# Kernel optimization log

Measured on AMD Instinct MI355X. Metric: run time of the kernel, lower is better.

Reference implementation:

```python
import jax, jax.numpy as jnp
from jax import lax
import numpy as np

# dims
V, D, T = 30000, 300, 24          # vocab, glove dim, seq len
H = 256                            # tweet_out_size == z_dim
NT, NU = 6000, 4000                # tweet nodes, user nodes
N = NT + NU
F, Z = 512, 256                    # user_feat_size, z_dim
E = 80000
B = 2000                           # batch_size (source tweets)
H1, H2, HEADS = 64, 100, 8
NEG = 0.2                          # GATConv default negative_slope


def setup_inputs() -> dict:
    k = jax.random.split(jax.random.key(0), 32)
    r = lambda i, shape, s=0.05: (s * jax.random.normal(k[i], shape)).astype(jnp.float32)
    return {
        "user_text": jax.random.randint(k[0], (B, T), 0, V),
        "user_feats": jax.random.normal(k[1], (NU, F), jnp.float32),
        "graph_node_features": jax.random.randint(k[2], (NT, T), 0, V),
        "graph_edge_index": jax.random.randint(k[3], (2, E), 0, N),
        "tweet_emb": r(4, (V, D), 0.1),
        "w_ih0": r(5, (3 * H, D)), "w_hh0": r(6, (3 * H, H)),
        "b_ih0": r(7, (3 * H,)), "b_hh0": r(8, (3 * H,)),
        "w_ih1": r(9, (3 * H, H)), "w_hh1": r(10, (3 * H, H)),
        "b_ih1": r(11, (3 * H,)), "b_hh1": r(12, (3 * H,)),
        "h0": r(13, (2, NT, H), 1.0),
        "w_mu": r(14, (Z, F)), "b_mu": r(15, (Z,)),
        "w_lv": r(16, (Z, F)), "b_lv": r(17, (Z,)),
        "w_dec": r(18, (F, Z)), "b_dec": r(19, (F,)),
        "vae_eps": r(20, (NU, Z), 1.0),
        "w1": r(21, (H, HEADS * H1)), "a_src1": r(22, (HEADS, H1)),
        "a_dst1": r(23, (HEADS, H1)), "b1": r(24, (HEADS * H1,)),
        "w2": r(25, (HEADS * H1, H2)), "a_src2": r(26, (1, H2)),
        "a_dst2": r(27, (1, H2)), "b2": r(28, (H2,)),
    }


def _gru_layer(x_seq, h0, w_ih, w_hh, b_ih, b_hh):
    # x_seq: [T, B, in]; torch nn.GRU gate math
    def step(h, x):
        gi = x @ w_ih.T + b_ih
        gh = h @ w_hh.T + b_hh
        i_r, i_z, i_n = jnp.split(gi, 3, axis=-1)
        h_r, h_z, h_n = jnp.split(gh, 3, axis=-1)
        r = jax.nn.sigmoid(i_r + h_r)
        z = jax.nn.sigmoid(i_z + h_z)
        n = jnp.tanh(i_n + r * h_n)
        hn = (1.0 - z) * n + z * h
        return hn, hn
    h_last, out = lax.scan(step, h0, x_seq)
    return out, h_last


def _gat(x, src, dst, w, a_src, a_dst, bias, heads, out_ch, concat):
    # PyG GATConv (eval mode, self-loops already appended)
    n = x.shape[0]
    xp = (x @ w).reshape(n, heads, out_ch)          # [N, H, C]
    as_n = (xp * a_src).sum(-1)                     # [N, H]
    ad_n = (xp * a_dst).sum(-1)
    e = jax.nn.leaky_relu(as_n[src] + ad_n[dst], NEG)          # [E, H]
    emax = jax.ops.segment_max(e, dst, num_segments=n)         # edge-softmax over dst
    ee = jnp.exp(e - emax[dst])
    denom = jax.ops.segment_sum(ee, dst, num_segments=n)
    alpha = ee / denom[dst]
    out = jax.ops.segment_sum(xp[src] * alpha[:, :, None], dst, num_segments=n)
    out = out.reshape(n, heads * out_ch) if concat else out.mean(axis=1)
    return out + bias


def reference(user_text, user_feats, graph_node_features, graph_edge_index,
              tweet_emb, w_ih0, w_hh0, b_ih0, b_hh0, w_ih1, w_hh1, b_ih1, b_hh1,
              h0, w_mu, b_mu, w_lv, b_lv, w_dec, b_dec, vae_eps,
              w1, a_src1, a_dst1, b1, w2, a_src2, a_dst2, b2):
    # --- VAE user embedding ---
    mu = user_feats @ w_mu.T + b_mu
    logvar = user_feats @ w_lv.T + b_lv
    z = mu + jnp.exp(0.5 * logvar) * vae_eps        # reparameterized latent
    rec = z @ w_dec.T + b_dec
    kl_loss = (-0.5 * (1.0 + logvar - mu**2 - jnp.exp(logvar)).sum(-1)).mean()
    rec_loss = ((rec - user_feats) ** 2).mean()
    # --- tweet encoder: embedding lookup + 2-layer GRU ---
    xe = tweet_emb[graph_node_features].transpose(1, 0, 2)     # [T, NT, D]
    out0, _ = _gru_layer(xe, h0[0], w_ih0, w_hh0, b_ih0, b_hh0)
    _, hn = _gru_layer(out0, h0[1], w_ih1, w_hh1, b_ih1, b_hh1)  # [NT, H]
    # --- assemble node features: source tweets, users, other tweets ---
    x_in = jnp.concatenate([hn[:B], z, hn[B:]], axis=0)        # [N, H]
    loops = jnp.arange(x_in.shape[0])
    src = jnp.concatenate([graph_edge_index[0], loops])
    dst = jnp.concatenate([graph_edge_index[1], loops])
    x1 = _gat(x_in, src, dst, w1, a_src1, a_dst1, b1, HEADS, H1, True)
    x2 = _gat(x1, src, dst, w2, a_src2, a_dst2, b2, 1, H2, False)
    return x2, kl_loss, rec_loss
```

## Files before the change

### kernel.cpp

```cpp
#include <hip/hip_runtime.h>

#define V_ 30000
#define D_ 300
#define DP_ 320
#define T_ 24
#define H_ 256
#define NT_ 6000
#define NU_ 4000
#define N_ 10000
#define F_ 512
#define Z_ 256
#define E_ 80000
#define B_ 2000
#define H1_ 64
#define H2_ 100
#define HEADS_ 8
#define E2_ (E_ + N_)

typedef __bf16 bf16_t;
typedef bf16_t bf16x8 __attribute__((ext_vector_type(8)));
typedef float  f32x4  __attribute__((ext_vector_type(4)));

__device__ __forceinline__ void gll16(const bf16_t* g, bf16_t* l)
{
    __builtin_amdgcn_global_load_lds(
        (const __attribute__((address_space(1))) void*)g,
        (__attribute__((address_space(3))) void*)l, 16, 0, 0);
}

struct GCfg {
    const bf16_t* A; const bf16_t* B; const float* bias;
    float* Cf; bf16_t* Cb; int M, N, K, ldc;
    const int* gtok; int t0;
};

template<bool OUTBF>
__global__ __launch_bounds__(256) void mfma_gemm(GCfg g0, GCfg g1)
{
    const GCfg g = blockIdx.z ? g1 : g0;
    __shared__ __align__(16) bf16_t SMEM[16384];
    const int tid  = (int)threadIdx.x;
    const int wave = tid >> 6, lane = tid & 63;
    const int quad = lane >> 4, l16 = lane & 15;
    const int mq = (wave & 1) * 64, nq = (wave >> 1) * 64;

    int bx = (int)blockIdx.x, by = (int)blockIdx.y;
    {
        int gx = (int)gridDim.x, total = gx * (int)gridDim.y;
        if ((total & 7) == 0) {
            int L = by * gx + bx;
            int F = (L & 7) * (total >> 3) + (L >> 3);
            bx = F % gx;
            by = F / gx;
        }
    }
    const int mbase = by * 128, nbase = bx * 128;
    const int M = g.M, N = g.N, K = g.K, ldc = g.ldc;

    const bf16_t* agp[2];
    const bf16_t* bgp[2];
#pragma unroll
    for (int j = 0; j < 2; j++) {
        int i = wave * 128 + j * 64 + lane;
        int c = i >> 7, row = i & 127;
        int r = mbase + row; if (r >= M) r = M - 1;
        int src = g.gtok ? g.gtok[(r % NT_) * T_ + g.t0 + (r / NT_)] : r;
        agp[j] = g.A + (size_t)src * K + c * 8;
        int rb = nbase + row; if (rb >= N) rb = N - 1;
        bgp[j] = g.B + (size_t)rb * K + c * 8;
    }

    f32x4 acc[4][4];
#pragma unroll
    for (int mi = 0; mi < 4; mi++)
#pragma unroll
        for (int ni = 0; ni < 4; ni++) acc[mi][ni] = (f32x4){0.f, 0.f, 0.f, 0.f};

    auto stage = [&](int b, int k0) {
        bf16_t* ab = SMEM + b * 4096 + wave * 1024;
        bf16_t* bb = SMEM + 8192 + b * 4096 + wave * 1024;
        gll16(agp[0] + k0, ab);
        gll16(agp[1] + k0, ab + 512);
        gll16(bgp[0] + k0, bb);
        gll16(bgp[1] + k0, bb + 512);
    };

    const int niter = K >> 5;
    stage(0, 0);
    for (int ks = 0; ks < niter; ks++) {
        __syncthreads();
        if (ks + 1 < niter) stage((ks + 1) & 1, (ks + 1) * 32);
        const bf16_t* Ab = SMEM + (ks & 1) * 4096;
        const bf16_t* Bb = SMEM + 8192 + (ks & 1) * 4096;
        bf16x8 afr[4], bfr[4];
#pragma unroll
        for (int mi = 0; mi < 4; mi++)
            afr[mi] = *(const bf16x8*)(Ab + (size_t)(quad * 128 + mq + mi * 16 + l16) * 8);
#pragma unroll
        for (int ni = 0; ni < 4; ni++)
            bfr[ni] = *(const bf16x8*)(Bb + (size_t)(quad * 128 + nq + ni * 16 + l16) * 8);
#pragma unroll
        for (int mi = 0; mi < 4; mi++)
#pragma unroll
            for (int ni = 0; ni < 4; ni++)
                acc[mi][ni] = __builtin_amdgcn_mfma_f32_16x16x32_bf16(
                    afr[mi], bfr[ni], acc[mi][ni], 0, 0, 0);
    }

    if (OUTBF) {
        __syncthreads();
#pragma unroll
        for (int ni = 0; ni < 4; ni++) {
            int colc = nq + ni * 16 + l16;
            float bv = g.bias ? g.bias[nbase + colc] : 0.f;
            int cc = colc >> 3, off = colc & 7;
#pragma unroll
            for (int mi = 0; mi < 4; mi++)
#pragma unroll
                for (int r = 0; r < 4; r++) {
                    int row = mq + mi * 16 + quad * 4 + r;
                    int sw = (row ^ (row >> 3)) & 7;
                    SMEM[row * 128 + ((cc ^ sw) << 3) + off] =
                        (bf16_t)(acc[mi][ni][r] + bv);
                }
        }
        __syncthreads();
        {
            int row = tid >> 1, seg = tid & 1;
            int sw = (row ^ (row >> 3)) & 7;
            int growr = mbase + row;
            if (growr < M) {
#pragma unroll
                for (int q = 0; q < 8; q++) {
                    int cc = seg * 8 + q;
                    bf16x8 v = *(const bf16x8*)(SMEM + row * 128 + ((cc ^ sw) << 3));
                    *(bf16x8*)(g.Cb + (size_t)growr * ldc + nbase + cc * 8) = v;
                }
            }
        }
    } else {
#pragma unroll
        for (int ni = 0; ni < 4; ni++) {
            int col = nbase + nq + ni * 16 + l16;
            if (col >= N) continue;
            float bv = g.bias ? g.bias[col] : 0.f;
#pragma unroll
            for (int mi = 0; mi < 4; mi++)
#pragma unroll
                for (int r = 0; r < 4; r++) {
                    int row = mbase + mq + mi * 16 + quad * 4 + r;
                    if (row >= M) continue;
                    g.Cf[(size_t)row * ldc + col] = acc[mi][ni][r] + bv;
                }
        }
    }
}

struct MegaLay {
    const bf16_t* temb;
    const int*    gnf;
    const bf16_t* wih0;
    const bf16_t* whh0;
    const bf16_t* wih1;
    const bf16_t* whh1;
    const float *bih0, *bhh0, *bih1, *bhh1;
    const bf16_t* h0in;
    const bf16_t* h1in;
    bf16_t*       h1out;
};

__device__ __forceinline__ float rcp_(float x)
{
    float r;
    asm("v_rcp_f32 %0, %1" : "=v"(r) : "v"(x));
    return r;
}
__device__ __forceinline__ float sigm_(float x)
{
    return rcp_(1.f + __expf(-x));
}
__device__ __forceinline__ float tanh_(float x)
{
    x = fminf(fmaxf(x, -15.f), 15.f);
    float t = __expf(2.f * x);
    return 1.f - 2.f * rcp_(t + 1.f);
}

#define HSW(Hb, row, byte) ((char*)(Hb) + ((((row) * 512) + (byte)) ^ (((row) & 7) << 4)))

__global__ __launch_bounds__(512, 2) void gru_mega(MegaLay L)
{
    __shared__ __align__(16) bf16_t H0L[8192];
    __shared__ __align__(16) bf16_t H1L[8192];
    __shared__ __align__(16) bf16_t XE[20480];
    __shared__ int TOK[768];
    const int tid  = (int)threadIdx.x;
    const int wv   = tid >> 6, lane = tid & 63;
    const int quad = lane >> 4, l16 = lane & 15;
    const int row0 = (int)blockIdx.x * 32;

    for (int i = tid; i < 768; i += 512) {
        int gi = row0 * T_ + i; if (gi >= NT_ * T_) gi = NT_ * T_ - 1;
        TOK[i] = L.gnf[gi];
    }
#pragma unroll
    for (int i = 0; i < 2; i++) {
        int idx  = i * 512 + tid;
        int rowl = idx >> 5, seg = idx & 31;
        int grow = row0 + rowl; if (grow >= NT_) grow = NT_ - 1;
        *(bf16x8*)HSW(H0L, rowl, seg * 16) =
            *(const bf16x8*)(L.h0in + (size_t)grow * H_ + seg * 8);
        *(bf16x8*)HSW(H1L, rowl, seg * 16) =
            *(const bf16x8*)(L.h1in + (size_t)grow * H_ + seg * 8);
    }

    float brz0[2][2], bni0[2], bnh0[2], brz1[2][2], bni1[2], bnh1[2];
#pragma unroll
    for (int jj = 0; jj < 2; jj++) {
        int col = wv * 32 + jj * 16 + l16;
        brz0[0][jj] = L.bih0[col] + L.bhh0[col];
        brz0[1][jj] = L.bih0[256 + col] + L.bhh0[256 + col];
        bni0[jj]    = L.bih0[512 + col];
        bnh0[jj]    = L.bhh0[512 + col];
        brz1[0][jj] = L.bih1[col] + L.bhh1[col];
        brz1[1][jj] = L.bih1[256 + col] + L.bhh1[256 + col];
        bni1[jj]    = L.bih1[512 + col];
        bnh1[jj]    = L.bhh1[512 + col];
    }

    auto gather = [&](int t) {
        bf16_t* xb = XE + (t & 1) * 10240;
#pragma unroll
        for (int k = 0; k < 3; k++) {
            int i = wv + k * 8;
            if (i < 20) {
                int flat = i * 64 + lane;
                int row  = flat / 40;
                int s    = flat - row * 40;
                int c4   = s ^ (row & 7);
                int tok  = TOK[row * T_ + t];
                gll16(L.temb + (size_t)tok * DP_ + c4 * 8, xb + i * 512 + lane * 8);
            }
        }
    };

    auto run_gemm = [&](auto&& loadA, const bf16_t* W, int nks,
                        f32x4 (&arz)[2][2][2], f32x4 (&an)[2][2]) {
#pragma unroll 2
        for (int ks = 0; ks < nks; ks++) {
            bf16x8 afr[2];
            loadA(afr, ks);
            bf16x8 bfr[3][2];
#pragma unroll
            for (int g = 0; g < 3; g++)
#pragma unroll
                for (int jj = 0; jj < 2; jj++)
                    bfr[g][jj] = *(const bf16x8*)(W +
                        (((size_t)(g * 16 + wv * 2 + jj) * nks + ks) << 9) + lane * 8);
#pragma unroll
            for (int m = 0; m < 2; m++)
#pragma unroll
                for (int jj = 0; jj < 2; jj++) {
                    arz[m][0][jj] = __builtin_amdgcn_mfma_f32_16x16x32_bf16(
                        afr[m], bfr[0][jj], arz[m][0][jj], 0, 0, 0);
                    arz[m][1][jj] = __builtin_amdgcn_mfma_f32_16x16x32_bf16(
                        afr[m], bfr[1][jj], arz[m][1][jj], 0, 0, 0);
                    an[m][jj] = __builtin_amdgcn_mfma_f32_16x16x32_bf16(
                        afr[m], bfr[2][jj], an[m][jj], 0, 0, 0);
                }
        }
    };

    __syncthreads();
    gather(0);

    for (int t = 0; t < T_; t++) {
        __syncthreads();
        if (t + 1 < T_) gather(t + 1);

        f32x4 arz[2][2][2], an_i[2][2], an_h[2][2];
#pragma unroll
        for (int m = 0; m < 2; m++)
#pragma unroll
            for (int jj = 0; jj < 2; jj++) {
                arz[m][0][jj] = (f32x4){0.f, 0.f, 0.f, 0.f};
                arz[m][1][jj] = (f32x4){0.f, 0.f, 0.f, 0.f};
                an_i[m][jj]   = (f32x4){0.f, 0.f, 0.f, 0.f};
                an_h[m][jj]   = (f32x4){0.f, 0.f, 0.f, 0.f};
            }

        {
            const bf16_t* xb = XE + (t & 1) * 10240;
            run_gemm([&](bf16x8* afr, int ks) {
#pragma unroll
                for (int m = 0; m < 2; m++) {
                    int row = m * 16 + l16;
                    afr[m] = *(const bf16x8*)(xb + row * DP_ +
                               (((ks * 4 + quad) ^ (row & 7)) << 3));
                }
            }, L.wih0, 10, arz, an_i);
            run_gemm([&](bf16x8* afr, int ks) {
#pragma unroll
                for (int m = 0; m < 2; m++)
                    afr[m] = *(const bf16x8*)HSW(H0L, m * 16 + l16,
                                                 ks * 64 + quad * 16);
            }, L.whh0, 8, arz, an_h);
        }
        __syncthreads();

#pragma unroll
        for (int m = 0; m < 2; m++)
#pragma unroll
            for (int jj = 0; jj < 2; jj++) {
                int col = wv * 32 + jj * 16 + l16;
#pragma unroll
                for (int r = 0; r < 4; r++) {
                    int rowl = m * 16 + quad * 4 + r;
                    float hold = (float)*(const bf16_t*)HSW(H0L, rowl, col * 2);
                    float rg = sigm_(arz[m][0][jj][r] + brz0[0][jj]);
                    float zg = sigm_(arz[m][1][jj][r] + brz0[1][jj]);
                    float ng = tanh_(an_i[m][jj][r] + bni0[jj] +
                                     rg * (an_h[m][jj][r] + bnh0[jj]));
                    *(bf16_t*)HSW(H0L, rowl, col * 2) =
                        (bf16_t)((1.f - zg) * ng + zg * hold);
                }
            }
        __syncthreads();

#pragma unroll
        for (int m = 0; m < 2; m++)
#pragma unroll
            for (int jj = 0; jj < 2; jj++) {
                arz[m][0][jj] = (f32x4){0.f, 0.f, 0.f, 0.f};
                arz[m][1][jj] = (f32x4){0.f, 0.f, 0.f, 0.f};
                an_i[m][jj]   = (f32x4){0.f, 0.f, 0.f, 0.f};
                an_h[m][jj]   = (f32x4){0.f, 0.f, 0.f, 0.f};
            }
        run_gemm([&](bf16x8* afr, int ks) {
#pragma unroll
            for (int m = 0; m < 2; m++)
                afr[m] = *(const bf16x8*)HSW(H0L, m * 16 + l16,
                                             ks * 64 + quad * 16);
        }, L.wih1, 8, arz, an_i);
        run_gemm([&](bf16x8* afr, int ks) {
#pragma unroll
            for (int m = 0; m < 2; m++)
                afr[m] = *(const bf16x8*)HSW(H1L, m * 16 + l16,
                                             ks * 64 + quad * 16);
        }, L.whh1, 8, arz, an_h);
        __syncthreads();

#pragma unroll
        for (int m = 0; m < 2; m++)
#pragma unroll
            for (int jj = 0; jj < 2; jj++) {
                int col = wv * 32 + jj * 16 + l16;
#pragma unroll
                for (int r = 0; r < 4; r++) {
                    int rowl = m * 16 + quad * 4 + r;
                    float hold = (float)*(const bf16_t*)HSW(H1L, rowl, col * 2);
                    float rg = sigm_(arz[m][0][jj][r] + brz1[0][jj]);
                    float zg = sigm_(arz[m][1][jj][r] + brz1[1][jj]);
                    float ng = tanh_(an_i[m][jj][r] + bni1[jj] +
                                     rg * (an_h[m][jj][r] + bnh1[jj]));
                    *(bf16_t*)HSW(H1L, rowl, col * 2) =
                        (bf16_t)((1.f - zg) * ng + zg * hold);
                }
            }
    }

    __syncthreads();
#pragma unroll
    for (int i = 0; i < 2; i++) {
        int idx  = i * 512 + tid;
        int rowl = idx >> 5, seg = idx & 31;
        int grow = row0 + rowl;
        if (grow < NT_) {
            bf16x8 v = *(const bf16x8*)HSW(H1L, rowl, seg * 16);
            *(bf16x8*)(L.h1out + (size_t)grow * H_ + seg * 8) = v;
        }
    }
}

struct SegD { const float* src; bf16_t* dst; int rows, cin, cout, transp; };
struct PrepArgs { SegD seg[11]; long long base[12]; int nseg; long long total; };

__global__ void prep_kern(PrepArgs pa)
{
    long long stride = (long long)gridDim.x * blockDim.x;
    for (long long i = (long long)blockIdx.x * blockDim.x + threadIdx.x;
         i < pa.total; i += stride) {
        int k = 0;
        while (k + 1 < pa.nseg && i >= pa.base[k + 1]) k++;
        long long local = i - pa.base[k];
        SegD sg = pa.seg[k];
        float v;
        if (sg.transp == 2) {
            int nks  = sg.cout >> 5;
            int o    = (int)local;
            int e    = o & 7;
            int lane = (o >> 3) & 63;
            int rest = o >> 9;
            int ks   = rest % nks;
            int gcb  = rest / nks;
            int r    = (gcb >> 4) * 256 + (gcb & 15) * 16 + (lane & 15);
            int kk   = ks * 32 + (lane >> 4) * 8 + e;
            v = (kk < sg.cin) ? sg.src[(size_t)r * sg.cin + kk] : 0.f;
        } else {
            int r = (int)(local / sg.cout);
            int c = (int)(local - (long long)r * sg.cout);
            if (sg.transp) v = sg.src[(size_t)c * sg.rows + r];
            else           v = (c < sg.cin) ? sg.src[(size_t)r * sg.cin + c] : 0.f;
        }
        sg.dst[local] = (bf16_t)v;
    }
}

__global__ void init_all(const float* __restrict__ h0in, bf16_t* __restrict__ h0b,
                         bf16_t* __restrict__ h1b,
                         int* __restrict__ deg, int* __restrict__ dcnt,
                         float* __restrict__ loss2, float* __restrict__ b_ml,
                         const float* __restrict__ b_mu, const float* __restrict__ b_lv)
{
    int i = blockIdx.x * blockDim.x + threadIdx.x;
    if (i < NT_ * H_) {
        h0b[i] = (bf16_t)h0in[i];
        h1b[i] = (bf16_t)h0in[NT_ * H_ + i];
    }
    if (i < N_) { deg[i] = 0; dcnt[i] = 0; }
    if (i < 2 * Z_) b_ml[i] = (i < Z_) ? b_mu[i] : b_lv[i - Z_];
    if (i < 2) loss2[i] = 0.f;
}

__device__ __forceinline__ void edge_sd(const int* __restrict__ ei, int e, int& s, int& d)
{
    if (e < E_) { s = ei[e]; d = ei[E_ + e]; }
    else        { s = d = e - E_; }
}

__global__ void csr_hist(const int* __restrict__ ei, int* __restrict__ deg)
{
    int e = blockIdx.x * blockDim.x + threadIdx.x;
    if (e >= E2_) return;
    int s, d; edge_sd(ei, e, s, d);
    atomicAdd(deg + d, 1);
}

__global__ void csr_scan(const int* __restrict__ deg, int* __restrict__ rowptr)
{
    __shared__ int buf[256];
    __shared__ int carry;
    int tid = (int)threadIdx.x;
    if (tid == 0) { carry = 0; rowptr[0] = 0; }
    __syncthreads();
    for (int c0 = 0; c0 < N_; c0 += 256) {
        int i = c0 + tid;
        buf[tid] = (i < N_) ? deg[i] : 0;
        __syncthreads();
        for (int off = 1; off < 256; off <<= 1) {
            int t = (tid >= off) ? buf[tid - off] : 0;
            __syncthreads();
            buf[tid] += t;
            __syncthreads();
        }
        if (i < N_) rowptr[i + 1] = carry + buf[tid];
        __syncthreads();
        if (tid == 255) carry += buf[255];
        __syncthreads();
    }
}

__global__ void csr_scatter(const int* __restrict__ ei, const int* __restrict__ rowptr,
                            int* __restrict__ dcnt, int* __restrict__ csrc)
{
    int e = blockIdx.x * blockDim.x + threadIdx.x;
    if (e >= E2_) return;
    int s, d; edge_sd(ei, e, s, d);
    int pos = rowptr[d] + atomicAdd(dcnt + d, 1);
    csrc[pos] = s;
}

__global__ __launch_bounds__(256) void vae_z_kl(
    const float* __restrict__ ml, const float* __restrict__ eps,
    bf16_t* __restrict__ z_out, float* __restrict__ kl_out)
{
    float t = 0.f;
    int stride = (int)gridDim.x * 256;
    for (int idx = blockIdx.x * 256 + threadIdx.x; idx < NU_ * Z_; idx += stride) {
        int row = idx >> 8, c = idx & 255;
        float m = ml[(size_t)row * 512 + c];
        float l = ml[(size_t)row * 512 + 256 + c];
        float el = expf(l);
        z_out[idx] = (bf16_t)(m + expf(0.5f * l) * eps[idx]);
        t += -0.5f * (1.f + l - m * m - el);
    }
    __shared__ float red[256];
    red[threadIdx.x] = t;
    __syncthreads();
    for (int s = 128; s > 0; s >>= 1) {
        if ((int)threadIdx.x < s) red[threadIdx.x] += red[threadIdx.x + s];
        __syncthreads();
    }
    if (threadIdx.x == 0) atomicAdd(kl_out, red[0] * (1.f / NU_));
}

__global__ __launch_bounds__(256) void rec_loss_kern(
    const float* __restrict__ rec, const float* __restrict__ uf,
    float* __restrict__ loss_out)
{
    float t = 0.f;
    int stride = (int)gridDim.x * 256;
    for (int idx = blockIdx.x * 256 + threadIdx.x; idx < NU_ * F_; idx += stride) {
        float d = rec[idx] - uf[idx];
        t += d * d;
    }
    __shared__ float red[256];
    red[threadIdx.x] = t;
    __syncthreads();
    for (int s = 128; s > 0; s >>= 1) {
        if ((int)threadIdx.x < s) red[threadIdx.x] += red[threadIdx.x + s];
        __syncthreads();
    }
    if (threadIdx.x == 0) atomicAdd(loss_out, red[0] * (1.f / (NU_ * F_)));
}

__global__ void assemble_xin(const bf16_t* __restrict__ h1, bf16_t* __restrict__ x_in)
{
    int idx = blockIdx.x * blockDim.x + threadIdx.x;
    if (idx >= NT_ * H_) return;
    int row = idx >> 8, col = idx & 255;
    int dst = (row < B_) ? row : (row + NU_);
    x_in[(size_t)dst * H_ + col] = h1[idx];
}

__global__ void gat_attn_coef_bf(const bf16_t* __restrict__ xp,
                                 const float* __restrict__ a_src,
                                 const float* __restrict__ a_dst,
                                 float* __restrict__ asn, float* __restrict__ adn,
                                 int heads, int C)
{
    int i = blockIdx.x * blockDim.x + threadIdx.x;
    if (i >= N_ * heads) return;
    int node = i / heads, h = i - node * heads;
    const bf16_t* x = xp + (size_t)(node * heads + h) * C;
    float s = 0.f, d = 0.f;
    for (int c8 = 0; c8 < C; c8 += 8) {
        bf16x8 v = *(const bf16x8*)(x + c8);
#pragma unroll
        for (int j = 0; j < 8; j++) {
            float vv = (float)v[j];
            s += vv * a_src[h * C + c8 + j];
            d += vv * a_dst[h * C + c8 + j];
        }
    }
    asn[i] = s;
    adn[i] = d;
}

__global__ void gat_attn_coef(const float* __restrict__ xp, const float* __restrict__ a_src,
                              const float* __restrict__ a_dst, float* __restrict__ asn,
                              float* __restrict__ adn, int heads, int C)
{
    int i = blockIdx.x * blockDim.x + threadIdx.x;
    if (i >= N_ * heads) return;
    int node = i / heads, h = i - node * heads;
    const float* x = xp + (size_t)(node * heads + h) * C;
    float s = 0.f, d = 0.f;
    for (int c = 0; c < C; c++) {
        float v = x[c];
        s += v * a_src[h * C + c];
        d += v * a_dst[h * C + c];
    }
    asn[i] = s;
    adn[i] = d;
}

__global__ __launch_bounds__(256) void gat_agg1(
    const int* __restrict__ rowptr, const int* __restrict__ csrc,
    const float* __restrict__ asn, const float* __restrict__ adn,
    const bf16_t* __restrict__ xp, const float* __restrict__ bias,
    bf16_t* __restrict__ x1out)
{
    int d = blockIdx.x;
    int tid = (int)threadIdx.x;
    int beg = rowptr[d], end = rowptr[d + 1];
    int h0 = tid >> 6, h1 = h0 + 4;
    float ad0 = adn[d * 8 + h0], ad1 = adn[d * 8 + h1];
    float mx0 = -1e30f, mx1 = -1e30f;
    for (int e = beg; e < end; e++) {
        int s = csrc[e];
        float l0 = asn[s * 8 + h0] + ad0; l0 = (l0 > 0.f) ? l0 : 0.2f * l0;
        float l1 = asn[s * 8 + h1] + ad1; l1 = (l1 > 0.f) ? l1 : 0.2f * l1;
        mx0 = fmaxf(mx0, l0); mx1 = fmaxf(mx1, l1);
    }
    float den0 = 0.f, den1 = 0.f, acc0 = 0.f, acc1 = 0.f;
    for (int e = beg; e < end; e++) {
        int s = csrc[e];
        float l0 = asn[s * 8 + h0] + ad0; l0 = (l0 > 0.f) ? l0 : 0.2f * l0;
        float l1 = asn[s * 8 + h1] + ad1; l1 = (l1 > 0.f) ? l1 : 0.2f * l1;
        float p0 = expf(l0 - mx0), p1 = expf(l1 - mx1);
        den0 += p0; den1 += p1;
        acc0 += p0 * (float)xp[(size_t)s * 512 + tid];
        acc1 += p1 * (float)xp[(size_t)s * 512 + 256 + tid];
    }
    x1out[(size_t)d * 512 + tid]       = (bf16_t)(bias[tid] + acc0 / den0);
    x1out[(size_t)d * 512 + 256 + tid] = (bf16_t)(bias[256 + tid] + acc1 / den1);
}

__global__ __launch_bounds__(256) void gat_agg2(
    const int* __restrict__ rowptr, const int* __restrict__ csrc,
    const float* __restrict__ asn, const float* __restrict__ adn,
    const float* __restrict__ xp, const float* __restrict__ bias,
    float* __restrict__ outp)
{
    int d = blockIdx.x * 4 + ((int)threadIdx.x >> 6);
    if (d >= N_) return;
    int lane = (int)threadIdx.x & 63;
    int beg = rowptr[d], end = rowptr[d + 1];
    float adnd = adn[d];
    float mx = -1e30f;
    for (int e = beg; e < end; e++) {
        float l = asn[csrc[e]] + adnd;
        l = (l > 0.f) ? l : 0.2f * l;
        mx = fmaxf(mx, l);
    }
    float den = 0.f, acc0 = 0.f, acc1 = 0.f;
    for (int e = beg; e < end; e++) {
        int s = csrc[e];
        float l = asn[s] + adnd;
        l = (l > 0.f) ? l : 0.2f * l;
        float p = expf(l - mx);
        den += p;
        acc0 += p * xp[(size_t)s * H2_ + lane];
        if (lane < H2_ - 64) acc1 += p * xp[(size_t)s * H2_ + 64 + lane];
    }
    outp[(size_t)d * H2_ + lane] = bias[lane] + acc0 / den;
    if (lane < H2_ - 64)
        outp[(size_t)d * H2_ + 64 + lane] = bias[64 + lane] + acc1 / den;
}

extern "C" void kernel_launch(void* const* d_in, const int* in_sizes, int n_in,
                              void* d_out, int out_size, void* d_ws, size_t ws_size,
                              hipStream_t stream)
{
    const float* user_feats = (const float*)d_in[1];
    const int*   gnf        = (const int*)d_in[2];
    const int*   ei         = (const int*)d_in[3];
    const float* temb       = (const float*)d_in[4];
    const float* w_ih0      = (const float*)d_in[5];
    const float* w_hh0      = (const float*)d_in[6];
    const float* b_ih0      = (const float*)d_in[7];
    const float* b_hh0      = (const float*)d_in[8];
    const float* w_ih1      = (const float*)d_in[9];
    const float* w_hh1      = (const float*)d_in[10];
    const float* b_ih1      = (const float*)d_in[11];
    const float* b_hh1      = (const float*)d_in[12];
    const float* h0in       = (const float*)d_in[13];
    const float* w_mu       = (const float*)d_in[14];
    const float* b_mu       = (const float*)d_in[15];
    const float* w_lv       = (const float*)d_in[16];
    const float* b_lv       = (const float*)d_in[17];
    const float* w_dec      = (const float*)d_in[18];
    const float* b_dec      = (const float*)d_in[19];
    const float* veps       = (const float*)d_in[20];
    const float* w1         = (const float*)d_in[21];
    const float* a_src1     = (const float*)d_in[22];
    const float* a_dst1     = (const float*)d_in[23];
    const float* b1         = (const float*)d_in[24];
    const float* w2         = (const float*)d_in[25];
    const float* a_src2     = (const float*)d_in[26];
    const float* a_dst2     = (const float*)d_in[27];
    const float* b2         = (const float*)d_in[28];
    float* out = (float*)d_out;

    char* wsb = (char*)d_ws;
    bf16_t* temb_bf = (bf16_t*)(wsb + 0);
    float*  mlbuf   = (float*)(wsb + 56064000);
    float*  recb    = (float*)(wsb + 64256000);
    bf16_t* xp1b    = (bf16_t*)(wsb + 0);
    bf16_t* x1b     = (bf16_t*)(wsb + 20480000);
    float*  xp2     = (float*)(wsb + 30720000);
    bf16_t* wih0_bf = (bf16_t*)(wsb + 92928000);
    bf16_t* whh0_bf = (bf16_t*)(wsb + 93419520);
    bf16_t* wih1_bf = (bf16_t*)(wsb + 93812736);
    bf16_t* whh1_bf = (bf16_t*)(wsb + 94205952);
    bf16_t* wml_bf  = (bf16_t*)(wsb + 94599168);
    bf16_t* wdec_bf = (bf16_t*)(wsb + 95123456);
    bf16_t* w1t_bf  = (bf16_t*)(wsb + 95385600);
    bf16_t* w2t_bf  = (bf16_t*)(wsb + 95648000);
    float*  b_ml    = (float*)(wsb + 95750400);
    bf16_t* ufeats_bf = (bf16_t*)(wsb + 95752448);
    bf16_t* h0b_init = (bf16_t*)(wsb + 124424448);
    bf16_t* h1init  = (bf16_t*)(wsb + 127496448);
    bf16_t* h1sA    = (bf16_t*)(wsb + 130568448);
    bf16_t* xin_bf  = (bf16_t*)(wsb + 136712448);
    int*    deg     = (int*)(wsb + 141832448);
    int*    dcnt    = (int*)(wsb + 141872448);
    int*    rowptr  = (int*)(wsb + 141912448);
    int*    csrc    = (int*)(wsb + 141952512);
    float*  asn1    = (float*)(wsb + 142312512);
    float*  adn1    = (float*)(wsb + 142632512);
    float*  asn2    = (float*)(wsb + 142952512);
    float*  adn2    = (float*)(wsb + 142992512);

    const int TB = 256;
    auto blocks = [](int n) { return (n + 255) / 256; };

    auto mkcfg = [](const bf16_t* A, const bf16_t* B, const float* bias,
                    float* Cf, bf16_t* Cb, int M, int N, int K, int ldc,
                    const int* gtok, int t0) {
        GCfg g; g.A = A; g.B = B; g.bias = bias; g.Cf = Cf; g.Cb = Cb;
        g.M = M; g.N = N; g.K = K; g.ldc = ldc; g.gtok = gtok; g.t0 = t0;
        return g;
    };
    auto launch_bf = [&](GCfg g0) {
        dim3 grid((g0.N + 127) / 128, (g0.M + 127) / 128, 1);
        hipLaunchKernelGGL((mfma_gemm<true>), grid, dim3(TB), 0, stream, g0, g0);
    };
    auto launch_f32 = [&](GCfg g0) {
        dim3 grid((g0.N + 127) / 128, (g0.M + 127) / 128, 1);
        hipLaunchKernelGGL((mfma_gemm<false>), grid, dim3(TB), 0, stream, g0, g0);
    };

    PrepArgs pa;
    auto seg = [&](int k, const float* s, bf16_t* dst, int rows, int cin, int cout, int tr) {
        pa.seg[k] = SegD{s, dst, rows, cin, cout, tr};
    };
    seg(0, temb, temb_bf, V_, D_, DP_, 0);
    seg(1, w_ih0, wih0_bf, 3 * H_, D_, DP_, 2);
    seg(2, w_hh0, whh0_bf, 3 * H_, H_, H_, 2);
    seg(3, w_ih1, wih1_bf, 3 * H_, H_, H_, 2);
    seg(4, w_hh1, whh1_bf, 3 * H_, H_, H_, 2);
    seg(5, w_mu, wml_bf, Z_, F_, F_, 0);
    seg(6, w_lv, wml_bf + (size_t)Z_ * F_, Z_, F_, F_, 0);
    seg(7, w_dec, wdec_bf, F_, Z_, Z_, 0);
    seg(8, user_feats, ufeats_bf, NU_, F_, F_, 0);
    seg(9, w1, w1t_bf, HEADS_ * H1_, 0, H_, 1);
    seg(10, w2, w2t_bf, H2_, 0, HEADS_ * H1_, 1);
    pa.nseg = 11;
    long long acc = 0;
    for (int k = 0; k < 11; k++) {
        pa.base[k] = acc;
        acc += (long long)pa.seg[k].rows * pa.seg[k].cout;
    }
    pa.base[11] = acc;
    pa.total = acc;
    hipLaunchKernelGGL(prep_kern, dim3(6144), dim3(TB), 0, stream, pa);

    hipLaunchKernelGGL(init_all, dim3(blocks(NT_ * H_)), dim3(TB), 0, stream,
                       h0in, h0b_init, h1init,
                       deg, dcnt, out + N_ * H2_, b_ml, b_mu, b_lv);

    hipLaunchKernelGGL(csr_hist, dim3(blocks(E2_)), dim3(TB), 0, stream, ei, deg);
    hipLaunchKernelGGL(csr_scan, dim3(1), dim3(TB), 0, stream, deg, rowptr);
    hipLaunchKernelGGL(csr_scatter, dim3(blocks(E2_)), dim3(TB), 0, stream,
                       ei, rowptr, dcnt, csrc);

    launch_f32(mkcfg(ufeats_bf, wml_bf, b_ml, mlbuf, nullptr,
                     NU_, 2 * Z_, F_, 2 * Z_, nullptr, 0));
    bf16_t* z_bf = xin_bf + (size_t)B_ * H_;
    hipLaunchKernelGGL(vae_z_kl, dim3(256), dim3(TB), 0, stream,
                       mlbuf, veps, z_bf, out + N_ * H2_);
    launch_f32(mkcfg(z_bf, wdec_bf, b_dec, recb, nullptr,
                     NU_, F_, Z_, F_, nullptr, 0));
    hipLaunchKernelGGL(rec_loss_kern, dim3(256), dim3(TB), 0, stream,
                       recb, user_feats, out + N_ * H2_ + 1);

    {
        MegaLay ML;
        ML.temb = temb_bf; ML.gnf = gnf;
        ML.wih0 = wih0_bf; ML.whh0 = whh0_bf;
        ML.wih1 = wih1_bf; ML.whh1 = whh1_bf;
        ML.bih0 = b_ih0; ML.bhh0 = b_hh0; ML.bih1 = b_ih1; ML.bhh1 = b_hh1;
        ML.h0in = h0b_init; ML.h1in = h1init; ML.h1out = h1sA;
        hipLaunchKernelGGL(gru_mega, dim3((NT_ + 31) / 32), dim3(512), 0, stream, ML);
    }

    hipLaunchKernelGGL(assemble_xin, dim3(blocks(NT_ * H_)), dim3(TB), 0, stream,
                       h1sA, xin_bf);

    launch_bf(mkcfg(xin_bf, w1t_bf, nullptr, nullptr, xp1b,
                    N_, HEADS_ * H1_, H_, HEADS_ * H1_, nullptr, 0));
    hipLaunchKernelGGL(gat_attn_coef_bf, dim3(blocks(N_ * HEADS_)), dim3(TB), 0, stream,
                       xp1b, a_src1, a_dst1, asn1, adn1, HEADS_, H1_);
    hipLaunchKernelGGL(gat_agg1, dim3(N_), dim3(TB), 0, stream,
                       rowptr, csrc, asn1, adn1, xp1b, b1, x1b);

    launch_f32(mkcfg(x1b, w2t_bf, nullptr, xp2, nullptr,
                     N_, H2_, HEADS_ * H1_, H2_, nullptr, 0));
    hipLaunchKernelGGL(gat_attn_coef, dim3(blocks(N_)), dim3(TB), 0, stream,
                       xp2, a_src2, a_dst2, asn2, adn2, 1, H2_);
    hipLaunchKernelGGL(gat_agg2, dim3((N_ + 3) / 4), dim3(TB), 0, stream,
                       rowptr, csrc, asn2, adn2, xp2, b2, out);

    (void)in_sizes; (void)n_in; (void)out_size; (void)ws_size;
}
```

Measured before the change: 855.7 us.

## Precompute layer-0 GRU input gates over the vocabulary instead of per timestep

Adds a GEMM that computes tweet_emb @ w_ih0^T + b_ih0 for all vocab entries up front, so the GRU mega-kernel gathers precomputed 768-wide gate rows per token instead of gathering embeddings into LDS and running a 300-wide input GEMM each step. This removes the per-step layer-0 input matmul (6000x24 rows) and the XE shared buffer, in exchange for a 30000-row GEMM and scattered 2-byte global gathers per element inside the recurrence. Launch bounds drop to 1 block per SM, presumably to give registers to the gi array, which may reduce latency hiding.

```diff
diff --git a/kernel.cpp b/kernel.cpp
--- a/kernel.cpp
+++ b/kernel.cpp
@@ -157,13 +157,12 @@
 }
 
 struct MegaLay {
-    const bf16_t* temb;
+    const bf16_t* vocGi;
     const int*    gnf;
-    const bf16_t* wih0;
     const bf16_t* whh0;
     const bf16_t* wih1;
     const bf16_t* whh1;
-    const float *bih0, *bhh0, *bih1, *bhh1;
+    const float *bhh0, *bih1, *bhh1;
     const bf16_t* h0in;
     const bf16_t* h1in;
     bf16_t*       h1out;
@@ -188,11 +187,10 @@
 
 #define HSW(Hb, row, byte) ((char*)(Hb) + ((((row) * 512) + (byte)) ^ (((row) & 7) << 4)))
 
-__global__ __launch_bounds__(512, 2) void gru_mega(MegaLay L)
+__global__ __launch_bounds__(512, 1) void gru_mega(MegaLay L)
 {
     __shared__ __align__(16) bf16_t H0L[8192];
     __shared__ __align__(16) bf16_t H1L[8192];
-    __shared__ __align__(16) bf16_t XE[20480];
     __shared__ int TOK[768];
     const int tid  = (int)threadIdx.x;
     const int wv   = tid >> 6, lane = tid & 63;
@@ -214,49 +212,32 @@
             *(const bf16x8*)(L.h1in + (size_t)grow * H_ + seg * 8);
     }
 
-    float brz0[2][2], bni0[2], bnh0[2], brz1[2][2], bni1[2], bnh1[2];
+    float bh0[3][2], brz1[2][2], bni1[2], bnh1[2];
 #pragma unroll
     for (int jj = 0; jj < 2; jj++) {
         int col = wv * 32 + jj * 16 + l16;
-        brz0[0][jj] = L.bih0[col] + L.bhh0[col];
-        brz0[1][jj] = L.bih0[256 + col] + L.bhh0[256 + col];
-        bni0[jj]    = L.bih0[512 + col];
-        bnh0[jj]    = L.bhh0[512 + col];
+        bh0[0][jj] = L.bhh0[col];
+        bh0[1][jj] = L.bhh0[256 + col];
+        bh0[2][jj] = L.bhh0[512 + col];
         brz1[0][jj] = L.bih1[col] + L.bhh1[col];
         brz1[1][jj] = L.bih1[256 + col] + L.bhh1[256 + col];
         bni1[jj]    = L.bih1[512 + col];
         bnh1[jj]    = L.bhh1[512 + col];
     }
 
-    auto gather = [&](int t) {
-        bf16_t* xb = XE + (t & 1) * 10240;
-#pragma unroll
-        for (int k = 0; k < 3; k++) {
-            int i = wv + k * 8;
-            if (i < 20) {
-                int flat = i * 64 + lane;
-                int row  = flat / 40;
-                int s    = flat - row * 40;
-                int c4   = s ^ (row & 7);
-                int tok  = TOK[row * T_ + t];
-                gll16(L.temb + (size_t)tok * DP_ + c4 * 8, xb + i * 512 + lane * 8);
-            }
-        }
-    };
-
-    auto run_gemm = [&](auto&& loadA, const bf16_t* W, int nks,
+    auto run_gemm = [&](auto&& loadA, const bf16_t* W,
                         f32x4 (&arz)[2][2][2], f32x4 (&an)[2][2]) {
 #pragma unroll 2
-        for (int ks = 0; ks < nks; ks++) {
+        for (int ks = 0; ks < 8; ks++) {
+            bf16x8 bfr[3][2];
+#pragma unroll
+            for (int g = 0; g < 3; g++)
+#pragma unroll
+                for (int jj = 0; jj < 2; jj++)
+                    bfr[g][jj] = *(const bf16x8*)(W +
+                        (((size_t)(g * 16 + wv * 2 + jj) * 8 + ks) << 9) + lane * 8);
             bf16x8 afr[2];
             loadA(afr, ks);
-            bf16x8 bfr[3][2];
-#pragma unroll
-            for (int g = 0; g < 3; g++)
-#pragma unroll
-                for (int jj = 0; jj < 2; jj++)
-                    bfr[g][jj] = *(const bf16x8*)(W +
-                        (((size_t)(g * 16 + wv * 2 + jj) * nks + ks) << 9) + lane * 8);
 #pragma unroll
             for (int m = 0; m < 2; m++)
 #pragma unroll
@@ -272,11 +253,24 @@
     };
 
     __syncthreads();
-    gather(0);
 
     for (int t = 0; t < T_; t++) {
-        __syncthreads();
-        if (t + 1 < T_) gather(t + 1);
+        float gi[2][2][4][3];
+#pragma unroll
+        for (int m = 0; m < 2; m++)
+#pragma unroll
+            for (int r2 = 0; r2 < 4; r2++) {
+                int rowl = m * 16 + quad * 4 + r2;
+                const bf16_t* gp = L.vocGi +
+                    (size_t)TOK[rowl * T_ + t] * (3 * H_);
+#pragma unroll
+                for (int jj = 0; jj < 2; jj++) {
+                    int col = wv * 32 + jj * 16 + l16;
+#pragma unroll
+                    for (int g = 0; g < 3; g++)
+                        gi[m][jj][r2][g] = (float)gp[g * 256 + col];
+                }
+            }
 
         f32x4 arz[2][2][2], an_i[2][2], an_h[2][2];
 #pragma unroll
@@ -285,27 +279,15 @@
             for (int jj = 0; jj < 2; jj++) {
                 arz[m][0][jj] = (f32x4){0.f, 0.f, 0.f, 0.f};
                 arz[m][1][jj] = (f32x4){0.f, 0.f, 0.f, 0.f};
-                an_i[m][jj]   = (f32x4){0.f, 0.f, 0.f, 0.f};
                 an_h[m][jj]   = (f32x4){0.f, 0.f, 0.f, 0.f};
             }
 
-        {
-            const bf16_t* xb = XE + (t & 1) * 10240;
-            run_gemm([&](bf16x8* afr, int ks) {
-#pragma unroll
-                for (int m = 0; m < 2; m++) {
-                    int row = m * 16 + l16;
-                    afr[m] = *(const bf16x8*)(xb + row * DP_ +
-                               (((ks * 4 + quad) ^ (row & 7)) << 3));
-                }
-            }, L.wih0, 10, arz, an_i);
-            run_gemm([&](bf16x8* afr, int ks) {
-#pragma unroll
-                for (int m = 0; m < 2; m++)
-                    afr[m] = *(const bf16x8*)HSW(H0L, m * 16 + l16,
-                                                 ks * 64 + quad * 16);
-            }, L.whh0, 8, arz, an_h);
-        }
+        run_gemm([&](bf16x8* afr, int ks) {
+#pragma unroll
+            for (int m = 0; m < 2; m++)
+                afr[m] = *(const bf16x8*)HSW(H0L, m * 16 + l16,
+                                             ks * 64 + quad * 16);
+        }, L.whh0, arz, an_h);
         __syncthreads();
 
 #pragma unroll
@@ -317,10 +299,10 @@
                 for (int r = 0; r < 4; r++) {
                     int rowl = m * 16 + quad * 4 + r;
                     float hold = (float)*(const bf16_t*)HSW(H0L, rowl, col * 2);
-                    float rg = sigm_(arz[m][0][jj][r] + brz0[0][jj]);
-                    float zg = sigm_(arz[m][1][jj][r] + brz0[1][jj]);
-                    float ng = tanh_(an_i[m][jj][r] + bni0[jj] +
-                                     rg * (an_h[m][jj][r] + bnh0[jj]));
+                    float rg = sigm_(gi[m][jj][r][0] + arz[m][0][jj][r] + bh0[0][jj]);
+                    float zg = sigm_(gi[m][jj][r][1] + arz[m][1][jj][r] + bh0[1][jj]);
+                    float ng = tanh_(gi[m][jj][r][2] +
+                                     rg * (an_h[m][jj][r] + bh0[2][jj]));
                     *(bf16_t*)HSW(H0L, rowl, col * 2) =
                         (bf16_t)((1.f - zg) * ng + zg * hold);
                 }
@@ -341,13 +323,13 @@
             for (int m = 0; m < 2; m++)
                 afr[m] = *(const bf16x8*)HSW(H0L, m * 16 + l16,
                                              ks * 64 + quad * 16);
-        }, L.wih1, 8, arz, an_i);
+        }, L.wih1, arz, an_i);
         run_gemm([&](bf16x8* afr, int ks) {
 #pragma unroll
             for (int m = 0; m < 2; m++)
                 afr[m] = *(const bf16x8*)HSW(H1L, m * 16 + l16,
                                              ks * 64 + quad * 16);
-        }, L.whh1, 8, arz, an_h);
+        }, L.whh1, arz, an_h);
         __syncthreads();
 
 #pragma unroll
@@ -675,8 +657,9 @@
 
     char* wsb = (char*)d_ws;
     bf16_t* temb_bf = (bf16_t*)(wsb + 0);
-    float*  mlbuf   = (float*)(wsb + 56064000);
-    float*  recb    = (float*)(wsb + 64256000);
+    bf16_t* vocGi   = (bf16_t*)(wsb + 19200000);
+    float*  mlbuf   = (float*)(wsb + 66000000);
+    float*  recb    = (float*)(wsb + 75000000);
     bf16_t* xp1b    = (bf16_t*)(wsb + 0);
     bf16_t* x1b     = (bf16_t*)(wsb + 20480000);
     float*  xp2     = (float*)(wsb + 30720000);
@@ -727,7 +710,7 @@
         pa.seg[k] = SegD{s, dst, rows, cin, cout, tr};
     };
     seg(0, temb, temb_bf, V_, D_, DP_, 0);
-    seg(1, w_ih0, wih0_bf, 3 * H_, D_, DP_, 2);
+    seg(1, w_ih0, wih0_bf, 3 * H_, D_, DP_, 0);
     seg(2, w_hh0, whh0_bf, 3 * H_, H_, H_, 2);
     seg(3, w_ih1, wih1_bf, 3 * H_, H_, H_, 2);
     seg(4, w_hh1, whh1_bf, 3 * H_, H_, H_, 2);
@@ -756,6 +739,9 @@
     hipLaunchKernelGGL(csr_scatter, dim3(blocks(E2_)), dim3(TB), 0, stream,
                        ei, rowptr, dcnt, csrc);
 
+    launch_bf(mkcfg(temb_bf, wih0_bf, b_ih0, nullptr, vocGi,
+                    V_, 3 * H_, DP_, 3 * H_, nullptr, 0));
+
     launch_f32(mkcfg(ufeats_bf, wml_bf, b_ml, mlbuf, nullptr,
                      NU_, 2 * Z_, F_, 2 * Z_, nullptr, 0));
     bf16_t* z_bf = xin_bf + (size_t)B_ * H_;
@@ -768,10 +754,9 @@
 
     {
         MegaLay ML;
-        ML.temb = temb_bf; ML.gnf = gnf;
-        ML.wih0 = wih0_bf; ML.whh0 = whh0_bf;
-        ML.wih1 = wih1_bf; ML.whh1 = whh1_bf;
-        ML.bih0 = b_ih0; ML.bhh0 = b_hh0; ML.bih1 = b_ih1; ML.bhh1 = b_hh1;
+        ML.vocGi = vocGi; ML.gnf = gnf;
+        ML.whh0 = whh0_bf; ML.wih1 = wih1_bf; ML.whh1 = whh1_bf;
+        ML.bhh0 = b_hh0; ML.bih1 = b_ih1; ML.bhh1 = b_hh1;
         ML.h0in = h0b_init; ML.h1in = h1init; ML.h1out = h1sA;
         hipLaunchKernelGGL(gru_mega, dim3((NT_ + 31) / 32), dim3(512), 0, stream, ML);
     }
```

Measured after the change: 835.8 us. 1.02x faster.
